# Performance work log

Hardware: AMD Instinct MI355X
Metric: run time of the kernel (lower is better)

The kernel has to match this reference:

```python
import jax, jax.numpy as jnp
import numpy as np

N, E, EDGES, G = 4096, 256, 131072, 64
H, DH = 4, 64  # MHA heads, head dim


def _ln(x, g, b, eps=1e-5):
    m = jnp.mean(x, -1, keepdims=True)
    v = jnp.var(x, -1, keepdims=True)
    return g * (x - m) * jax.lax.rsqrt(v + eps) + b


def setup_inputs() -> dict:
    key = jax.random.key(0)
    ks = jax.random.split(key, 40)
    i = iter(range(40))
    def rn(shape, s=1.0):
        return jax.random.normal(ks[next(i)], shape, jnp.float32) * s
    w = lambda shape: rn(shape, 0.02)
    inp = {
        "node_hidden": rn((N, E)),
        "edge_hidden": rn((EDGES, E)),
        "pos": rn((N, 3)),
        # GINEConv MLP: Lin(E,2E) -> LN -> ReLU -> Dropout -> Lin(2E,E)
        "gine_w1": w((E, 2 * E)), "gine_b1": jnp.zeros((2 * E,)),
        "gine_ln_g": jnp.ones((2 * E,)), "gine_ln_b": jnp.zeros((2 * E,)),
        "gine_w2": w((2 * E, E)), "gine_b2": jnp.zeros((E,)),
        "norm1_g": jnp.ones((E,)), "norm1_b": jnp.zeros((E,)),
        # DirectionalMessagePassing params
        "dir_w": w((3, E)), "dir_b": jnp.zeros((E,)),
        "msg_w": w((E, E)), "msg_b": jnp.zeros((E,)),
        # MultiheadAttention
        "wq": w((E, E)), "bq": jnp.zeros((E,)),
        "wk": w((E, E)), "bk": jnp.zeros((E,)),
        "wv": w((E, E)), "bv": jnp.zeros((E,)),
        "wo": w((E, E)), "bo": jnp.zeros((E,)),
        # gate
        "gate_w": w((2 * E, E)), "gate_b": jnp.zeros((E,)),
        "norm2_g": jnp.ones((E,)), "norm2_b": jnp.zeros((E,)),
        # GraphNorm affine
        "gn_g": jnp.ones((E,)), "gn_b": jnp.zeros((E,)),
        # int inputs
        "edge_index": jax.random.randint(ks[next(i)], (2, EDGES), 0, N, jnp.int64 if jax.config.jax_enable_x64 else jnp.int32),
        "node_id": jnp.sort(jax.random.randint(ks[next(i)], (N,), 0, G)),
        "edge_id": jax.random.randint(ks[next(i)], (EDGES,), 0, G),
    }
    return inp


def reference(node_hidden, edge_hidden, pos,
              gine_w1, gine_b1, gine_ln_g, gine_ln_b, gine_w2, gine_b2,
              norm1_g, norm1_b, dir_w, dir_b, msg_w, msg_b,
              wq, bq, wk, bk, wv, bv, wo, bo,
              gate_w, gate_b, norm2_g, norm2_b, gn_g, gn_b,
              edge_index, node_id, edge_id):
    src, dst = edge_index[0], edge_index[1]
    identity = node_hidden

    # --- GINEConv: out = MLP(x + sum_j relu(x_j + e_ij)), eps=0 ---
    msg = jax.nn.relu(node_hidden[src] + edge_hidden)           # [EDGES, E]
    agg = jax.ops.segment_sum(msg, dst, num_segments=N)         # [N, E]
    h = node_hidden + agg
    h = jax.nn.relu(_ln(h @ gine_w1 + gine_b1, gine_ln_g, gine_ln_b))
    gnn_out = _ln(h @ gine_w2 + gine_b2, norm1_g, norm1_b)      # norm1

    # --- DirectionalMessagePassing over unit edge directions ---
    vec = pos[dst] - pos[src]                                   # [EDGES, 3]
    vec = vec / (jnp.linalg.norm(vec, axis=-1, keepdims=True) + 1e-8)
    dfeat = vec @ dir_w + dir_b                                 # [EDGES, E]
    smsg = gnn_out[src] * dfeat
    sagg = jax.ops.segment_sum(smsg, dst, num_segments=N)
    spatial_out = sagg @ msg_w + msg_b                          # [N, E]

    # --- MHA: q = gnn_out, k = v = spatial_out (seq = nodes, batch=1) ---
    q = (gnn_out @ wq + bq).reshape(N, H, DH)
    k = (spatial_out @ wk + bk).reshape(N, H, DH)
    v = (spatial_out @ wv + bv).reshape(N, H, DH)
    scores = jnp.einsum("nhd,mhd->hnm", q, k) / np.sqrt(DH)
    attn = jax.nn.softmax(scores, axis=-1)
    fused = jnp.einsum("hnm,mhd->nhd", attn, v).reshape(N, E) @ wo + bo

    # --- gated residual blend + norm2 ---
    gate = jax.nn.sigmoid(jnp.concatenate([fused, identity], -1) @ gate_w + gate_b)
    out = gate * fused + (1.0 - gate) * identity
    out = _ln(out, norm2_g, norm2_b)

    # --- GraphNorm: per-graph mean/var over nodes (segment stats) ---
    counts = jax.ops.segment_sum(jnp.ones((N, 1), out.dtype), node_id, num_segments=G)
    mean = jax.ops.segment_sum(out, node_id, num_segments=G) / counts
    cen = out - mean[node_id]
    var = jax.ops.segment_sum(cen * cen, node_id, num_segments=G) / counts
    out = gn_g * cen * jax.lax.rsqrt(var[node_id] + 1e-5) + gn_b

    # last_act = True; dropout is eval-mode identity
    return jax.nn.relu(out)
```

## Files before the change

kernel.cpp:

```cpp
#include <hip/hip_runtime.h>
#include <hip/hip_bf16.h>

#define N_NODES 4096
#define E_DIM   256
#define N_EDGES 131072
#define N_GRAPHS 64
#define H_HEADS 4
#define DH      64
#define SPLIT   4

typedef unsigned short u16;
typedef __attribute__((ext_vector_type(8))) short bf16x8;
typedef __attribute__((ext_vector_type(4))) float f32x4;

__device__ __forceinline__ float u2f(u16 u) {
    union { unsigned int i; float f; } c; c.i = ((unsigned int)u) << 16; return c.f;
}
__device__ __forceinline__ u16 f2bu(float f) {
    __hip_bfloat16 h = __float2bfloat16(f);
    return *reinterpret_cast<u16*>(&h);
}
__device__ __forceinline__ float ldv(const void* p, size_t i, int f32) {
    return f32 ? ((const float*)p)[i] : u2f(((const u16*)p)[i]);
}
__device__ __forceinline__ float4 ldv4(const void* p, size_t i, int f32) {
    if (f32) return *(const float4*)((const float*)p + i);
    ushort4 u = *(const ushort4*)((const u16*)p + i);
    return make_float4(u2f(u.x), u2f(u.y), u2f(u.z), u2f(u.w));
}
__device__ __forceinline__ float4 ldb4(const u16* p, size_t i) {
    ushort4 u = *(const ushort4*)(p + i);
    return make_float4(u2f(u.x), u2f(u.y), u2f(u.z), u2f(u.w));
}
__device__ __forceinline__ int chk_f32(const void* ones_raw) { return ((const u16*)ones_raw)[0] == 0; }
__device__ __forceinline__ int chk_i64(const int* ei) {
    return (ei[1] == 0 && ei[3] == 0 && ei[5] == 0 && ei[7] == 0);
}
__device__ __forceinline__ int ldi(const int* p, int i, int i64) {
    return i64 ? p[2 * i] : p[i];
}

struct SmDesc { const void* src; float* dst; int n; };
struct SmTable { SmDesc d[18]; };
struct WtDesc { const void* src; u16* dst; int K; int N; int base; };
struct WtTable { WtDesc d[8]; };

__global__ __launch_bounds__(256) void k_prep(const void* __restrict__ x_r, float* __restrict__ xf,
                                              u16* __restrict__ xh, const void* __restrict__ pos_r,
                                              float4* __restrict__ pos4, SmTable st, WtTable wt,
                                              const void* __restrict__ msgw_r, u16* __restrict__ msgwb,
                                              const void* __restrict__ wo_r, u16* __restrict__ wob,
                                              const void* __restrict__ ones_raw) {
    __shared__ u16 tile[64][68];
    int b = blockIdx.x, t = threadIdx.x;
    int f32 = chk_f32(ones_raw);
    if (b < 4096) {
        int i = b * 256 + t;
        float v = ldv(x_r, i, f32);
        xf[i] = v; xh[i] = f2bu(v);
        return;
    }
    b -= 4096;
    if (b < 16) {
        int n = b * 256 + t;
        pos4[n] = make_float4(ldv(pos_r, n * 3 + 0, f32), ldv(pos_r, n * 3 + 1, f32),
                              ldv(pos_r, n * 3 + 2, f32), 0.f);
        return;
    }
    b -= 16;
    if (b < 18 * 48) {
        int ti = b / 48;
        int off = (b % 48) * 256 + t;
        SmDesc e = st.d[ti];
        if (off < e.n) e.dst[off] = ldv(e.src, off, f32);
        return;
    }
    b -= 18 * 48;
    if (b < 160) {
        int i = 0;
        while (i < 7 && b >= wt.d[i + 1].base) i++;
        WtDesc e = wt.d[i];
        int tl = b - e.base;
        int ntn = e.N >> 6;
        int kt = tl / ntn, nt = tl % ntn;
        int r = t >> 2, c0 = (t & 3) * 16;
#pragma unroll
        for (int j = 0; j < 16; j++)
            tile[r][c0 + j] = f2bu(ldv(e.src, (size_t)(kt * 64 + r) * e.N + nt * 64 + c0 + j, f32));
        __syncthreads();
#pragma unroll
        for (int j = 0; j < 16; j++)
            e.dst[(size_t)(nt * 64 + r) * e.K + kt * 64 + c0 + j] = tile[c0 + j][r];
        return;
    }
    b -= 160;
    if (b < 256) { int i = b * 256 + t; msgwb[i] = f2bu(ldv(msgw_r, i, f32)); return; }
    b -= 256;
    { int i = b * 256 + t; wob[i] = f2bu(ldv(wo_r, i, f32)); }
}

__global__ __launch_bounds__(256) void k_asm2(const u16* __restrict__ wot, const u16* __restrict__ foldT,
                                              const u16* __restrict__ gwt, u16* __restrict__ BT2) {
    int idx = blockIdx.x * 256 + threadIdx.x;
    int col = idx >> 9, k = idx & 511;
    u16 v;
    if (col < 256) v = (k < 256) ? wot[col * 256 + k] : (u16)0;
    else { int c = col - 256; v = (k < 256) ? foldT[c * 256 + k] : gwt[(size_t)c * 512 + k]; }
    BT2[idx] = v;
}

__global__ __launch_bounds__(256) void k_biases(const float* __restrict__ bqf, const float* __restrict__ bkf,
                                                const float* __restrict__ bvf, const float* __restrict__ msgbf,
                                                const u16* __restrict__ wkvt, const float* __restrict__ bof,
                                                const float* __restrict__ gbf, const u16* __restrict__ gwt,
                                                float* __restrict__ bqkv, float* __restrict__ bias2) {
    int b = blockIdx.x, t = threadIdx.x;
    if (b < 3) {
        int i = b * 256 + t;
        if (i < 256) { bqkv[i] = bqf[i]; return; }
        int c = i - 256;
        float s = (c < 256) ? bkf[c] : bvf[c - 256];
        const u16* row = wkvt + (size_t)c * 256;
        float acc = 0.f;
        for (int k = 0; k < 256; k++) acc = fmaf(msgbf[k], u2f(row[k]), acc);
        bqkv[256 + c] = s + acc;
    } else if (b == 3) {
        bias2[t] = bof[t];
    } else {
        float acc = gbf[t];
        const u16* row = gwt + (size_t)t * 512;
        for (int j = 0; j < 256; j++) acc = fmaf(bof[j], u2f(row[j]), acc);
        bias2[256 + t] = acc;
    }
}

__global__ __launch_bounds__(256) void k_mgemm(const void* __restrict__ A0, const void* __restrict__ A1,
                                               int as0, int as1, int abf0, int abf1,
                                               int K0, int Ktot, const u16* __restrict__ BT,
                                               const float* __restrict__ bias, void* __restrict__ C,
                                               int Nc, int outbf, int mode, u16* __restrict__ vt) {
    __shared__ u16 As[64 * 64];
    __shared__ u16 Bs[64 * 64];
    int t = threadIdx.x;
    int wv = t >> 6, l = t & 63, lg = l >> 4, lc = l & 15;
    int wm = wv >> 1, wn = wv & 1;
    int m0 = blockIdx.y * 64, n0 = blockIdx.x * 64;
    f32x4 acc[2][2] = {};
    int sr = t >> 2, sc = (t & 3) * 16;
    int sw = (sr & 7) << 3;

    for (int k0 = 0; k0 < Ktot; k0 += 64) {
        const void* Ab; int astr, kof, abf;
        if (mode == 1) { int pick = (n0 < K0); Ab = pick ? A0 : A1; astr = pick ? as0 : as1; abf = pick ? abf0 : abf1; kof = k0; }
        else if (k0 < K0) { Ab = A0; astr = as0; abf = abf0; kof = k0; }
        else { Ab = A1; astr = as1; abf = abf1; kof = k0 - K0; }
        if (abf) {
            const u16* Ap = (const u16*)Ab + (size_t)(m0 + sr) * astr + kof + sc;
            *(bf16x8*)&As[(sr * 64 + sc) ^ sw]     = *(const bf16x8*)Ap;
            *(bf16x8*)&As[(sr * 64 + sc + 8) ^ sw] = *(const bf16x8*)(Ap + 8);
        } else {
            const float* Ap = (const float*)Ab + (size_t)(m0 + sr) * astr + kof + sc;
#pragma unroll
            for (int j = 0; j < 2; j++) {
                float4 f0 = *(const float4*)(Ap + j * 8);
                float4 f1 = *(const float4*)(Ap + j * 8 + 4);
                bf16x8 bv;
                bv[0] = (short)f2bu(f0.x); bv[1] = (short)f2bu(f0.y);
                bv[2] = (short)f2bu(f0.z); bv[3] = (short)f2bu(f0.w);
                bv[4] = (short)f2bu(f1.x); bv[5] = (short)f2bu(f1.y);
                bv[6] = (short)f2bu(f1.z); bv[7] = (short)f2bu(f1.w);
                *(bf16x8*)&As[(sr * 64 + sc + j * 8) ^ sw] = bv;
            }
        }
        const u16* Bp = BT + (size_t)(n0 + sr) * Ktot + k0 + sc;
        *(bf16x8*)&Bs[(sr * 64 + sc) ^ sw]     = *(const bf16x8*)Bp;
        *(bf16x8*)&Bs[(sr * 64 + sc + 8) ^ sw] = *(const bf16x8*)(Bp + 8);
        __syncthreads();
#pragma unroll
        for (int ks = 0; ks < 2; ks++) {
            bf16x8 af[2], bfr[2];
#pragma unroll
            for (int mi = 0; mi < 2; mi++) {
                int row = wm * 32 + mi * 16 + lc;
                af[mi] = *(const bf16x8*)&As[(row * 64 + ks * 32 + lg * 8) ^ ((row & 7) << 3)];
            }
#pragma unroll
            for (int ni = 0; ni < 2; ni++) {
                int col = wn * 32 + ni * 16 + lc;
                bfr[ni] = *(const bf16x8*)&Bs[(col * 64 + ks * 32 + lg * 8) ^ ((col & 7) << 3)];
            }
#pragma unroll
            for (int mi = 0; mi < 2; mi++)
#pragma unroll
                for (int ni = 0; ni < 2; ni++)
                    acc[mi][ni] = __builtin_amdgcn_mfma_f32_16x16x32_bf16(af[mi], bfr[ni], acc[mi][ni], 0, 0, 0);
        }
        __syncthreads();
    }
#pragma unroll
    for (int mi = 0; mi < 2; mi++)
#pragma unroll
        for (int ni = 0; ni < 2; ni++) {
            int col = n0 + wn * 32 + ni * 16 + lc;
            float bb = bias ? bias[col] : 0.f;
#pragma unroll
            for (int r = 0; r < 4; r++) {
                int row = m0 + wm * 32 + mi * 16 + lg * 4 + r;
                float v = acc[mi][ni][r] + bb;
                u16 hb = f2bu(v);
                if (outbf) ((u16*)C)[(size_t)row * Nc + col] = hb;
                else       ((float*)C)[(size_t)row * Nc + col] = v;
                if (vt && col >= 512) vt[(size_t)(col - 512) * N_NODES + row] = hb;
            }
        }
}

__global__ __launch_bounds__(256) void k_attn(const u16* __restrict__ QKV, const u16* __restrict__ VT,
                                              u16* __restrict__ part) {
    __shared__ u16 K_lds[64 * 64];
    __shared__ u16 V_lds[64 * 64];
    __shared__ u16 P_lds[4][16 * 64];
    int t = threadIdx.x;
    int wv = t >> 6, l = t & 63;
    int lg = l >> 4, lc = l & 15;
    int h = blockIdx.y, c = blockIdx.z;
    int q0 = blockIdx.x * 64 + wv * 16;

    bf16x8 qf[2];
#pragma unroll
    for (int kk = 0; kk < 2; kk++)
        qf[kk] = *(const bf16x8*)&QKV[(size_t)(q0 + lc) * 768 + h * DH + kk * 32 + lg * 8];

    f32x4 oacc[4] = {};
    float mrow[4], lrow[4];
#pragma unroll
    for (int r = 0; r < 4; r++) { mrow[r] = -1e30f; lrow[r] = 0.f; }

    int lr = t >> 2, lc16 = (t & 3) * 16;

    for (int kv0 = c * (N_NODES / SPLIT); kv0 < (c + 1) * (N_NODES / SPLIT); kv0 += 64) {
        __syncthreads();
        {
            int base = lr * 64 + lc16;
            int sw = (lr & 7) << 3;
            const u16* kp = &QKV[(size_t)(kv0 + lr) * 768 + 256 + h * DH + lc16];
            *(bf16x8*)&K_lds[(base) ^ sw]     = *(const bf16x8*)kp;
            *(bf16x8*)&K_lds[(base + 8) ^ sw] = *(const bf16x8*)(kp + 8);
            const u16* vp = &VT[((size_t)h * DH + lr) * N_NODES + kv0 + lc16];
            *(bf16x8*)&V_lds[(base) ^ sw]     = *(const bf16x8*)vp;
            *(bf16x8*)&V_lds[(base + 8) ^ sw] = *(const bf16x8*)(vp + 8);
        }
        __syncthreads();

        f32x4 s[4];
#pragma unroll
        for (int n = 0; n < 4; n++) {
            f32x4 a = {};
#pragma unroll
            for (int kk = 0; kk < 2; kk++) {
                int row = n * 16 + lc;
                bf16x8 b = *(const bf16x8*)&K_lds[(row * 64 + kk * 32 + lg * 8) ^ ((row & 7) << 3)];
                a = __builtin_amdgcn_mfma_f32_16x16x32_bf16(qf[kk], b, a, 0, 0, 0);
            }
            s[n] = a;
        }
        float tm[4];
#pragma unroll
        for (int r = 0; r < 4; r++) {
#pragma unroll
            for (int n = 0; n < 4; n++) s[n][r] *= 0.125f;
            tm[r] = fmaxf(fmaxf(s[0][r], s[1][r]), fmaxf(s[2][r], s[3][r]));
        }
#pragma unroll
        for (int msk = 1; msk < 16; msk <<= 1)
#pragma unroll
            for (int r = 0; r < 4; r++) tm[r] = fmaxf(tm[r], __shfl_xor(tm[r], msk));

        float p[4][4], psum[4];
#pragma unroll
        for (int r = 0; r < 4; r++) {
            float nm = fmaxf(mrow[r], tm[r]);
            float alpha = __expf(mrow[r] - nm);
            lrow[r] *= alpha;
#pragma unroll
            for (int n = 0; n < 4; n++) oacc[n][r] *= alpha;
            float ps = 0.f;
#pragma unroll
            for (int n = 0; n < 4; n++) { p[n][r] = __expf(s[n][r] - nm); ps += p[n][r]; }
            psum[r] = ps;
            mrow[r] = nm;
        }
#pragma unroll
        for (int msk = 1; msk < 16; msk <<= 1)
#pragma unroll
            for (int r = 0; r < 4; r++) psum[r] += __shfl_xor(psum[r], msk);
#pragma unroll
        for (int r = 0; r < 4; r++) lrow[r] += psum[r];

#pragma unroll
        for (int r = 0; r < 4; r++) {
            int q = lg * 4 + r;
            int sw = (q & 7) << 3;
#pragma unroll
            for (int n = 0; n < 4; n++)
                P_lds[wv][(q * 64 + n * 16 + lc) ^ sw] = f2bu(p[n][r]);
        }
#pragma unroll
        for (int kc = 0; kc < 2; kc++) {
            bf16x8 a = *(const bf16x8*)&P_lds[wv][(lc * 64 + kc * 32 + lg * 8) ^ ((lc & 7) << 3)];
#pragma unroll
            for (int n = 0; n < 4; n++) {
                int row = n * 16 + lc;
                bf16x8 b = *(const bf16x8*)&V_lds[(row * 64 + kc * 32 + lg * 8) ^ ((row & 7) << 3)];
                oacc[n] = __builtin_amdgcn_mfma_f32_16x16x32_bf16(a, b, oacc[n], 0, 0, 0);
            }
        }
    }

#pragma unroll
    for (int r = 0; r < 4; r++) {
        u16* pp = part + ((size_t)(c * H_HEADS + h) * N_NODES + q0 + lg * 4 + r) * 72;
#pragma unroll
        for (int n = 0; n < 4; n++) pp[n * 16 + lc] = f2bu(oacc[n][r]);
        if (lc == 0) { *(float*)(pp + 64) = mrow[r]; *(float*)(pp + 66) = lrow[r]; }
    }
}

__global__ __launch_bounds__(256) void k_combine(const u16* __restrict__ part, u16* __restrict__ attnoh) {
    int n = blockIdx.x, t = threadIdx.x;
    int h = t >> 6, d = t & 63;
    float M = -1e30f;
#pragma unroll
    for (int c = 0; c < SPLIT; c++)
        M = fmaxf(M, *(const float*)(part + ((size_t)(c * H_HEADS + h) * N_NODES + n) * 72 + 64));
    float L = 0.f, o = 0.f;
#pragma unroll
    for (int c = 0; c < SPLIT; c++) {
        const u16* pp = part + ((size_t)(c * H_HEADS + h) * N_NODES + n) * 72;
        float w = __expf(*(const float*)(pp + 64) - M);
        L = fmaf(*(const float*)(pp + 66), w, L);
        o = fmaf(u2f(pp[d]), w, o);
    }
    attnoh[(size_t)n * E_DIM + h * DH + d] = f2bu(o / L);
}

__device__ __forceinline__ void block_red2(float& a, float& b, float* sbuf) {
#pragma unroll
    for (int o = 32; o > 0; o >>= 1) { a += __shfl_down(a, o); b += __shfl_down(b, o); }
    int w = threadIdx.x >> 6;
    if ((threadIdx.x & 63) == 0) { sbuf[w] = a; sbuf[4 + w] = b; }
    __syncthreads();
    a = sbuf[0] + sbuf[1] + sbuf[2] + sbuf[3];
    b = sbuf[4] + sbuf[5] + sbuf[6] + sbuf[7];
    __syncthreads();
}

__global__ void k_count(const int* __restrict__ ei, int* __restrict__ count) {
    int e = blockIdx.x * 256 + threadIdx.x;
    int i64 = chk_i64(ei);
    int d = i64 ? ei[2 * (N_EDGES + e)] : ei[N_EDGES + e];
    atomicAdd(&count[d], 1);
}

__global__ __launch_bounds__(1024) void k_scan(const int* __restrict__ count,
                                               int* __restrict__ offs, int* __restrict__ cursor) {
    __shared__ int wsum[16];
    int t = threadIdx.x, lane = t & 63, wid = t >> 6;
    int c0 = count[t * 4 + 0], c1 = count[t * 4 + 1], c2 = count[t * 4 + 2], c3 = count[t * 4 + 3];
    int tot = c0 + c1 + c2 + c3;
    int inc = tot;
#pragma unroll
    for (int o = 1; o < 64; o <<= 1) { int v = __shfl_up(inc, o); if (lane >= o) inc += v; }
    if (lane == 63) wsum[wid] = inc;
    __syncthreads();
    if (t < 16) {
        int v = wsum[t];
#pragma unroll
        for (int o = 1; o < 16; o <<= 1) { int u = __shfl_up(v, o); if (t >= o) v += u; }
        wsum[t] = v;
    }
    __syncthreads();
    int base = (wid ? wsum[wid - 1] : 0) + inc - tot;
    int o0 = base, o1 = base + c0, o2 = o1 + c1, o3 = o2 + c2;
    offs[t * 4 + 0] = o0; offs[t * 4 + 1] = o1; offs[t * 4 + 2] = o2; offs[t * 4 + 3] = o3;
    cursor[t * 4 + 0] = o0; cursor[t * 4 + 1] = o1; cursor[t * 4 + 2] = o2; cursor[t * 4 + 3] = o3;
    if (t == 1023) offs[4096] = wsum[15];
}

__global__ void k_scatter(const int* __restrict__ ei, int* __restrict__ cursor,
                          int2* __restrict__ elist2) {
    int e = blockIdx.x * 256 + threadIdx.x;
    int i64 = chk_i64(ei);
    int s = i64 ? ei[2 * e] : ei[e];
    int d = i64 ? ei[2 * (N_EDGES + e)] : ei[N_EDGES + e];
    int p = atomicAdd(&cursor[d], 1);
    elist2[p] = make_int2(e, s);
}

__global__ __launch_bounds__(256) void k_gine_agg(const float* __restrict__ xf, const u16* __restrict__ xh,
                                                  const void* __restrict__ eh, const void* __restrict__ ones_raw,
                                                  const int* __restrict__ offs, const int2* __restrict__ elist2,
                                                  u16* __restrict__ houth) {
    int wv = threadIdx.x >> 6, ld = threadIdx.x & 63;
    int n = blockIdx.x * 4 + wv;
    int f32 = chk_f32(ones_raw);
    int cc = ld * 4;
    float4 acc = *(const float4*)&xf[(size_t)n * E_DIM + cc];
    int i0 = offs[n], i1 = offs[n + 1];
    int i = i0;
    for (; i + 4 <= i1; i += 4) {
        int2 es[4];
#pragma unroll
        for (int j = 0; j < 4; j++) es[j] = elist2[i + j];
        float4 a[4], x[4];
#pragma unroll
        for (int j = 0; j < 4; j++) a[j] = ldv4(eh, (size_t)es[j].x * E_DIM + cc, f32);
#pragma unroll
        for (int j = 0; j < 4; j++) x[j] = ldb4(xh, (size_t)es[j].y * E_DIM + cc);
#pragma unroll
        for (int j = 0; j < 4; j++) {
            acc.x += fmaxf(x[j].x + a[j].x, 0.f);
            acc.y += fmaxf(x[j].y + a[j].y, 0.f);
            acc.z += fmaxf(x[j].z + a[j].z, 0.f);
            acc.w += fmaxf(x[j].w + a[j].w, 0.f);
        }
    }
    for (; i < i1; i++) {
        int2 es = elist2[i];
        float4 a0 = ldv4(eh, (size_t)es.x * E_DIM + cc, f32);
        float4 x0 = ldb4(xh, (size_t)es.y * E_DIM + cc);
        acc.x += fmaxf(x0.x + a0.x, 0.f);
        acc.y += fmaxf(x0.y + a0.y, 0.f);
        acc.z += fmaxf(x0.z + a0.z, 0.f);
        acc.w += fmaxf(x0.w + a0.w, 0.f);
    }
    ushort4 o;
    o.x = f2bu(acc.x); o.y = f2bu(acc.y); o.z = f2bu(acc.z); o.w = f2bu(acc.w);
    *(ushort4*)&houth[(size_t)n * E_DIM + cc] = o;
}

template <int W, int OUTBF>
__global__ __launch_bounds__(256) void k_ln(const float* __restrict__ in, void* __restrict__ out,
                                            const float* __restrict__ g, const float* __restrict__ b,
                                            int relu) {
    __shared__ float sbuf[8];
    constexpr int PE = W / 256;
    int n = blockIdx.x, t = threadIdx.x;
    const float* row = in + (size_t)n * W;
    float x[PE];
    float s = 0.f, s2 = 0.f;
#pragma unroll
    for (int i = 0; i < PE; i++) { x[i] = row[t + i * 256]; s += x[i]; s2 += x[i] * x[i]; }
    block_red2(s, s2, sbuf);
    float mean = s / W;
    float var = fmaxf(s2 / W - mean * mean, 0.f);
    float rstd = rsqrtf(var + 1e-5f);
#pragma unroll
    for (int i = 0; i < PE; i++) {
        int c = t + i * 256;
        float y = g[c] * (x[i] - mean) * rstd + b[c];
        if (relu) y = fmaxf(y, 0.f);
        if (OUTBF) ((u16*)out)[(size_t)n * W + c] = f2bu(y);
        else       ((float*)out)[(size_t)n * W + c] = y;
    }
}

__global__ __launch_bounds__(256) void k_dir(const float4* __restrict__ pos4, const int* __restrict__ offs,
                                             const int2* __restrict__ elist2, const u16* __restrict__ gnnh,
                                             const float* __restrict__ dw, const float* __restrict__ db,
                                             u16* __restrict__ saggh) {
    int wv = threadIdx.x >> 6, ld = threadIdx.x & 63;
    int n = blockIdx.x * 4 + wv;
    int cc = ld * 4;
    float4 w0 = *(const float4*)&dw[cc];
    float4 w1 = *(const float4*)&dw[256 + cc];
    float4 w2 = *(const float4*)&dw[512 + cc];
    float4 bb = *(const float4*)&db[cc];
    float4 pn = pos4[n];
    float4 acc = {0.f, 0.f, 0.f, 0.f};
    int i0 = offs[n], i1 = offs[n + 1];
    int i = i0;
    for (; i + 2 <= i1; i += 2) {
        int2 es0 = elist2[i], es1 = elist2[i + 1];
        float4 p0 = pos4[es0.y], p1 = pos4[es1.y];
        float4 g0 = ldb4(gnnh, (size_t)es0.y * E_DIM + cc);
        float4 g1 = ldb4(gnnh, (size_t)es1.y * E_DIM + cc);
        float vx0 = pn.x - p0.x, vy0 = pn.y - p0.y, vz0 = pn.z - p0.z;
        float vx1 = pn.x - p1.x, vy1 = pn.y - p1.y, vz1 = pn.z - p1.z;
        float rn0 = 1.f / (sqrtf(vx0 * vx0 + vy0 * vy0 + vz0 * vz0) + 1e-8f);
        float rn1 = 1.f / (sqrtf(vx1 * vx1 + vy1 * vy1 + vz1 * vz1) + 1e-8f);
        acc.x = fmaf(g0.x, bb.x + (vx0 * w0.x + vy0 * w1.x + vz0 * w2.x) * rn0, acc.x);
        acc.y = fmaf(g0.y, bb.y + (vx0 * w0.y + vy0 * w1.y + vz0 * w2.y) * rn0, acc.y);
        acc.z = fmaf(g0.z, bb.z + (vx0 * w0.z + vy0 * w1.z + vz0 * w2.z) * rn0, acc.z);
        acc.w = fmaf(g0.w, bb.w + (vx0 * w0.w + vy0 * w1.w + vz0 * w2.w) * rn0, acc.w);
        acc.x = fmaf(g1.x, bb.x + (vx1 * w0.x + vy1 * w1.x + vz1 * w2.x) * rn1, acc.x);
        acc.y = fmaf(g1.y, bb.y + (vx1 * w0.y + vy1 * w1.y + vz1 * w2.y) * rn1, acc.y);
        acc.z = fmaf(g1.z, bb.z + (vx1 * w0.z + vy1 * w1.z + vz1 * w2.z) * rn1, acc.z);
        acc.w = fmaf(g1.w, bb.w + (vx1 * w0.w + vy1 * w1.w + vz1 * w2.w) * rn1, acc.w);
    }
    if (i < i1) {
        int2 es0 = elist2[i];
        float4 p0 = pos4[es0.y];
        float4 g0 = ldb4(gnnh, (size_t)es0.y * E_DIM + cc);
        float vx0 = pn.x - p0.x, vy0 = pn.y - p0.y, vz0 = pn.z - p0.z;
        float rn0 = 1.f / (sqrtf(vx0 * vx0 + vy0 * vy0 + vz0 * vz0) + 1e-8f);
        acc.x = fmaf(g0.x, bb.x + (vx0 * w0.x + vy0 * w1.x + vz0 * w2.x) * rn0, acc.x);
        acc.y = fmaf(g0.y, bb.y + (vx0 * w0.y + vy0 * w1.y + vz0 * w2.y) * rn0, acc.y);
        acc.z = fmaf(g0.z, bb.z + (vx0 * w0.z + vy0 * w1.z + vz0 * w2.z) * rn0, acc.z);
        acc.w = fmaf(g0.w, bb.w + (vx0 * w0.w + vy0 * w1.w + vz0 * w2.w) * rn0, acc.w);
    }
    ushort4 o;
    o.x = f2bu(acc.x); o.y = f2bu(acc.y); o.z = f2bu(acc.z); o.w = f2bu(acc.w);
    *(ushort4*)&saggh[(size_t)n * E_DIM + cc] = o;
}

__global__ __launch_bounds__(256) void k_gate_ln(const float* __restrict__ fg, const float* __restrict__ xf,
                                                 const float* __restrict__ g2, const float* __restrict__ b2,
                                                 float* __restrict__ out2) {
    __shared__ float sbuf[8];
    int n = blockIdx.x, t = threadIdx.x;
    float fu = fg[(size_t)n * 512 + t];
    float z  = fg[(size_t)n * 512 + 256 + t];
    float gate = 1.f / (1.f + __expf(-z));
    float o = gate * fu + (1.f - gate) * xf[(size_t)n * E_DIM + t];
    float s = o, s2 = o * o;
    block_red2(s, s2, sbuf);
    float mean = s / E_DIM;
    float var = fmaxf(s2 / E_DIM - mean * mean, 0.f);
    float y = g2[t] * (o - mean) * rsqrtf(var + 1e-5f) + b2[t];
    out2[(size_t)n * E_DIM + t] = y;
}

__device__ __forceinline__ int lbound(const int* __restrict__ nid, int v, int i64) {
    int lo = 0, hi = N_NODES;
    while (lo < hi) { int mid = (lo + hi) >> 1; if (ldi(nid, mid, i64) < v) lo = mid + 1; else hi = mid; }
    return lo;
}

__global__ __launch_bounds__(256) void k_gnstats(const int* __restrict__ nid, const int* __restrict__ ei,
                                                 const float* __restrict__ out2,
                                                 float* __restrict__ gnm, float* __restrict__ gnr) {
    int g = blockIdx.x, t = threadIdx.x;
    int i64 = chk_i64(ei);
    int a = lbound(nid, g, i64), bnd = lbound(nid, g + 1, i64);
    int cnt = bnd - a;
    float s = 0.f, s2 = 0.f;
    for (int n = a; n < bnd; n++) {
        float x = out2[(size_t)n * E_DIM + t];
        s += x; s2 = fmaf(x, x, s2);
    }
    float inv = cnt ? 1.f / (float)cnt : 0.f;
    float mean = s * inv;
    float var = fmaxf(s2 * inv - mean * mean, 0.f);
    gnm[g * E_DIM + t] = mean;
    gnr[g * E_DIM + t] = rsqrtf(var + 1e-5f);
}

__global__ __launch_bounds__(256) void k_gnapply(const float* __restrict__ out2, const int* __restrict__ nid,
                                                 const int* __restrict__ ei, const void* __restrict__ ones_raw,
                                                 const float* __restrict__ gnm, const float* __restrict__ gnr,
                                                 const float* __restrict__ gg, const float* __restrict__ gb,
                                                 void* __restrict__ out) {
    int n = blockIdx.x, t = threadIdx.x;
    int g = ldi(nid, n, chk_i64(ei));
    float y = gg[t] * (out2[(size_t)n * E_DIM + t] - gnm[g * E_DIM + t]) * gnr[g * E_DIM + t] + gb[t];
    y = fmaxf(y, 0.f);
    size_t idx = (size_t)n * E_DIM + t;
    if (chk_f32(ones_raw)) ((float*)out)[idx] = y;
    else ((__hip_bfloat16*)out)[idx] = __float2bfloat16(y);
}

extern "C" void kernel_launch(void* const* d_in, const int* in_sizes, int n_in,
                              void* d_out, int out_size, void* d_ws, size_t ws_size,
                              hipStream_t stream) {
    const void* x_r    = d_in[0];
    const void* eh_r   = d_in[1];
    const void* pos_r  = d_in[2];
    const void* w1_r   = d_in[3];
    const void* b1_r   = d_in[4];
    const void* glng_r = d_in[5];
    const void* glnb_r = d_in[6];
    const void* w2_r   = d_in[7];
    const void* b2_r   = d_in[8];
    const void* n1g_r  = d_in[9];
    const void* n1b_r  = d_in[10];
    const void* dirw_r = d_in[11];
    const void* dirb_r = d_in[12];
    const void* msgw_r = d_in[13];
    const void* msgb_r = d_in[14];
    const void* wq_r   = d_in[15];
    const void* bq_r   = d_in[16];
    const void* wk_r   = d_in[17];
    const void* bk_r   = d_in[18];
    const void* wv_r   = d_in[19];
    const void* bv_r   = d_in[20];
    const void* wo_r   = d_in[21];
    const void* bo_r   = d_in[22];
    const void* gw_r   = d_in[23];
    const void* gb_r   = d_in[24];
    const void* n2g_r  = d_in[25];
    const void* n2b_r  = d_in[26];
    const void* gng_r  = d_in[27];
    const void* gnb_r  = d_in[28];
    const int* ei      = (const int*)d_in[29];
    const int* nid     = (const int*)d_in[30];

    char* ws = (char*)d_ws;
    const size_t KB = 1 << 10, MB = 1 << 20;
    int*   count  = (int*)(ws + 0);
    int*   offs   = (int*)(ws + 32 * KB);
    int*   cursor = (int*)(ws + 64 * KB);
    int2*  elist2 = (int2*)(ws + 128 * KB);

    float* prm    = (float*)(ws + 1 * MB + 192 * KB);
    float* b1f   = prm + 0;
    float* glngf = prm + 512,  *glnbf = prm + 1024;
    float* b2f   = prm + 1536;
    float* n1gf  = prm + 1792, *n1bf  = prm + 2048;
    float* dirwf = prm + 2304;
    float* dirbf = prm + 3072, *msgbf = prm + 3328;
    float* bqf   = prm + 3584, *bkf   = prm + 3840, *bvf = prm + 4096, *bof = prm + 4352;
    float* gbf   = prm + 4608;
    float* n2gf  = prm + 4864, *n2bf  = prm + 5120;
    float* gngf  = prm + 5376, *gnbf  = prm + 5632;
    float4* pos4 = (float4*)(ws + 1 * MB + 256 * KB);

    u16* w1t    = (u16*)(ws + 2 * MB);
    u16* w2t    = (u16*)(ws + 2 * MB + 256 * KB);
    u16* wot    = (u16*)(ws + 2 * MB + 512 * KB);
    u16* gwt    = (u16*)(ws + 2 * MB + 640 * KB);
    u16* wqkvt  = (u16*)(ws + 3 * MB);
    u16* wkvt   = (u16*)(ws + 3 * MB + 384 * KB);
    u16* msgwb  = (u16*)(ws + 3 * MB + 640 * KB);
    u16* wob    = (u16*)(ws + 3 * MB + 768 * KB);
    u16* foldT  = (u16*)(ws + 3 * MB + 896 * KB);
    u16* BT2    = (u16*)(ws + 4 * MB);
    float* bias2f = (float*)(ws + 4 * MB + 512 * KB);
    float* bqkvf  = (float*)(ws + 4 * MB + 516 * KB);

    float* xf     = (float*)(ws + 5 * MB);
    u16*   xh     = (u16*)(ws + 9 * MB);
    u16*   hbufh  = (u16*)(ws + 11 * MB);
    float* T1     = (float*)(ws + 13 * MB);
    float* gnnf   = (float*)(ws + 21 * MB);
    u16*   gnnh   = (u16*)(ws + 25 * MB);
    u16*   saggh  = (u16*)(ws + 27 * MB);
    u16*   QKVh   = (u16*)(ws + 29 * MB);
    u16*   VT     = (u16*)(ws + 35 * MB);
    u16*   part   = (u16*)(ws + 37 * MB);
    u16*   attnoh = (u16*)(ws + 11 * MB);
    float* fg     = (float*)(ws + 13 * MB);
    float* out2   = (float*)(ws + 21 * MB);
    float* gnm    = (float*)(ws + 25 * MB);
    float* gnr    = (float*)(ws + 25 * MB + 64 * KB);

    SmTable st;
    {
        int i = 0;
        auto add = [&](const void* s, float* d, int n) { st.d[i].src = s; st.d[i].dst = d; st.d[i].n = n; i++; };
        add(b1_r, b1f, 512); add(glng_r, glngf, 512); add(glnb_r, glnbf, 512);
        add(b2_r, b2f, 256); add(n1g_r, n1gf, 256); add(n1b_r, n1bf, 256);
        add(dirw_r, dirwf, 768); add(dirb_r, dirbf, 256); add(msgb_r, msgbf, 256);
        add(bq_r, bqf, 256); add(bk_r, bkf, 256); add(bv_r, bvf, 256); add(bo_r, bof, 256);
        add(gb_r, gbf, 256); add(n2g_r, n2gf, 256); add(n2b_r, n2bf, 256);
        add(gng_r, gngf, 256); add(gnb_r, gnbf, 256);
    }
    WtTable wt;
    {
        int i = 0, base = 0;
        auto add = [&](const void* s, u16* d, int K, int N) {
            wt.d[i].src = s; wt.d[i].dst = d; wt.d[i].K = K; wt.d[i].N = N; wt.d[i].base = base;
            base += (K / 64) * (N / 64); i++;
        };
        add(w1_r, w1t, 256, 512);
        add(w2_r, w2t, 512, 256);
        add(wq_r, wqkvt, 256, 256);
        add(wk_r, wkvt, 256, 256);
        add(wv_r, wkvt + 256 * 256, 256, 256);
        add(wo_r, wot, 256, 256);
        add(gw_r, gwt, 512, 256);
        wt.d[7].base = 0x7fffffff;
    }
    k_prep<<<4096 + 16 + 18 * 48 + 160 + 256 + 256, 256, 0, stream>>>(
        x_r, xf, xh, pos_r, pos4, st, wt, msgw_r, msgwb, wo_r, wob, glng_r);

    hipMemsetAsync(count, 0, N_NODES * sizeof(int), stream);
    k_count<<<N_EDGES / 256, 256, 0, stream>>>(ei, count);
    k_scan<<<1, 1024, 0, stream>>>(count, offs, cursor);
    k_scatter<<<N_EDGES / 256, 256, 0, stream>>>(ei, cursor, elist2);

    k_mgemm<<<dim3(4, 8), 256, 0, stream>>>(wkvt, nullptr, 256, 0, 1, 0, 256, 256, msgwb,
                                            nullptr, wqkvt + 256 * 256, 256, 1, 0, nullptr);
    k_mgemm<<<dim3(4, 4), 256, 0, stream>>>(gwt, nullptr, 512, 0, 1, 0, 256, 256, wob,
                                            nullptr, foldT, 256, 1, 0, nullptr);
    k_asm2<<<1024, 256, 0, stream>>>(wot, foldT, gwt, BT2);
    k_biases<<<5, 256, 0, stream>>>(bqf, bkf, bvf, msgbf, wkvt, bof, gbf, gwt, bqkvf, bias2f);

    k_gine_agg<<<N_NODES / 4, 256, 0, stream>>>(xf, xh, eh_r, glng_r, offs, elist2, hbufh);
    k_mgemm<<<dim3(8, 64), 256, 0, stream>>>(hbufh, nullptr, 256, 0, 1, 0, 256, 256, w1t,
                                             b1f, T1, 512, 0, 0, nullptr);
    k_ln<512, 0><<<N_NODES, 256, 0, stream>>>(T1, T1, glngf, glnbf, 1);
    k_mgemm<<<dim3(4, 64), 256, 0, stream>>>(T1, nullptr, 512, 0, 0, 0, 512, 512, w2t,
                                             b2f, gnnf, 256, 0, 0, nullptr);
    k_ln<256, 1><<<N_NODES, 256, 0, stream>>>(gnnf, gnnh, n1gf, n1bf, 0);

    k_dir<<<N_NODES / 4, 256, 0, stream>>>(pos4, offs, elist2, gnnh, dirwf, dirbf, saggh);

    k_mgemm<<<dim3(12, 64), 256, 0, stream>>>(gnnh, saggh, 256, 256, 1, 1, 256, 256, wqkvt,
                                              bqkvf, QKVh, 768, 1, 1, VT);

    k_attn<<<dim3(N_NODES / 64, H_HEADS, SPLIT), 256, 0, stream>>>(QKVh, VT, part);
    k_combine<<<N_NODES, 256, 0, stream>>>(part, attnoh);

    k_mgemm<<<dim3(8, 64), 256, 0, stream>>>(attnoh, xf, 256, 256, 1, 0, 256, 512, BT2,
                                             bias2f, fg, 512, 0, 0, nullptr);
    k_gate_ln<<<N_NODES, 256, 0, stream>>>(fg, xf, n2gf, n2bf, out2);

    k_gnstats<<<N_GRAPHS, 256, 0, stream>>>(nid, ei, out2, gnm, gnr);
    k_gnapply<<<N_NODES, 256, 0, stream>>>(out2, nid, ei, glng_r, gnm, gnr, gngf, gnbf, d_out);
}
```

Baseline: 269.4 us.

## Restructure attention softmax, split GraphNorm stats, and merge small setup launches

The attention kernel swaps the MFMA operand order so each lane holds a full query column. Row max and sum then reduce with two shuffles instead of four, and the softmax uses exp2 with log2e folded into the scale. GraphNorm statistics are split into 8 chunks per graph, giving 512 blocks in place of 64, and the apply kernel sums the partials itself. The count memset is folded into the prep kernel, and the asm2 and biases kernels are merged into one launch, which cuts launch overhead at the cost of extra per-node partial reads.

Result: faster. 262.7 us (-2.5%).

```diff
diff --git a/kernel.cpp b/kernel.cpp
--- a/kernel.cpp
+++ b/kernel.cpp
@@ -50,7 +50,7 @@
                                               float4* __restrict__ pos4, SmTable st, WtTable wt,
                                               const void* __restrict__ msgw_r, u16* __restrict__ msgwb,
                                               const void* __restrict__ wo_r, u16* __restrict__ wob,
-                                              const void* __restrict__ ones_raw) {
+                                              int* __restrict__ count, const void* __restrict__ ones_raw) {
     __shared__ u16 tile[64][68];
     int b = blockIdx.x, t = threadIdx.x;
     int f32 = chk_f32(ones_raw);
@@ -96,25 +96,29 @@
     b -= 160;
     if (b < 256) { int i = b * 256 + t; msgwb[i] = f2bu(ldv(msgw_r, i, f32)); return; }
     b -= 256;
-    { int i = b * 256 + t; wob[i] = f2bu(ldv(wo_r, i, f32)); }
-}
-
-__global__ __launch_bounds__(256) void k_asm2(const u16* __restrict__ wot, const u16* __restrict__ foldT,
-                                              const u16* __restrict__ gwt, u16* __restrict__ BT2) {
-    int idx = blockIdx.x * 256 + threadIdx.x;
-    int col = idx >> 9, k = idx & 511;
-    u16 v;
-    if (col < 256) v = (k < 256) ? wot[col * 256 + k] : (u16)0;
-    else { int c = col - 256; v = (k < 256) ? foldT[c * 256 + k] : gwt[(size_t)c * 512 + k]; }
-    BT2[idx] = v;
-}
-
-__global__ __launch_bounds__(256) void k_biases(const float* __restrict__ bqf, const float* __restrict__ bkf,
-                                                const float* __restrict__ bvf, const float* __restrict__ msgbf,
-                                                const u16* __restrict__ wkvt, const float* __restrict__ bof,
-                                                const float* __restrict__ gbf, const u16* __restrict__ gwt,
-                                                float* __restrict__ bqkv, float* __restrict__ bias2) {
+    if (b < 256) { int i = b * 256 + t; wob[i] = f2bu(ldv(wo_r, i, f32)); return; }
+    b -= 256;
+    count[b * 256 + t] = 0;
+}
+
+__global__ __launch_bounds__(256) void k_post(const u16* __restrict__ wot, const u16* __restrict__ foldT,
+                                              const u16* __restrict__ gwt, u16* __restrict__ BT2,
+                                              const float* __restrict__ bqf, const float* __restrict__ bkf,
+                                              const float* __restrict__ bvf, const float* __restrict__ msgbf,
+                                              const u16* __restrict__ wkvt, const float* __restrict__ bof,
+                                              const float* __restrict__ gbf,
+                                              float* __restrict__ bqkv, float* __restrict__ bias2) {
     int b = blockIdx.x, t = threadIdx.x;
+    if (b < 1024) {
+        int idx = b * 256 + t;
+        int col = idx >> 9, k = idx & 511;
+        u16 v;
+        if (col < 256) v = (k < 256) ? wot[col * 256 + k] : (u16)0;
+        else { int c = col - 256; v = (k < 256) ? foldT[c * 256 + k] : gwt[(size_t)c * 512 + k]; }
+        BT2[idx] = v;
+        return;
+    }
+    b -= 1024;
     if (b < 3) {
         int i = b * 256 + t;
         if (i < 256) { bqkv[i] = bqf[i]; return; }
@@ -225,6 +229,7 @@
     int lg = l >> 4, lc = l & 15;
     int h = blockIdx.y, c = blockIdx.z;
     int q0 = blockIdx.x * 64 + wv * 16;
+    const float SC = 0.18033688f;
 
     bf16x8 qf[2];
 #pragma unroll
@@ -232,11 +237,10 @@
         qf[kk] = *(const bf16x8*)&QKV[(size_t)(q0 + lc) * 768 + h * DH + kk * 32 + lg * 8];
 
     f32x4 oacc[4] = {};
-    float mrow[4], lrow[4];
-#pragma unroll
-    for (int r = 0; r < 4; r++) { mrow[r] = -1e30f; lrow[r] = 0.f; }
+    float mx = -1e30f, lsum = 0.f;
 
     int lr = t >> 2, lc16 = (t & 3) * 16;
+    int swp = (lc & 7) << 3;
 
     for (int kv0 = c * (N_NODES / SPLIT); kv0 < (c + 1) * (N_NODES / SPLIT); kv0 += 64) {
         __syncthreads();
@@ -259,55 +263,46 @@
 #pragma unroll
             for (int kk = 0; kk < 2; kk++) {
                 int row = n * 16 + lc;
-                bf16x8 b = *(const bf16x8*)&K_lds[(row * 64 + kk * 32 + lg * 8) ^ ((row & 7) << 3)];
-                a = __builtin_amdgcn_mfma_f32_16x16x32_bf16(qf[kk], b, a, 0, 0, 0);
+                bf16x8 kf = *(const bf16x8*)&K_lds[(row * 64 + kk * 32 + lg * 8) ^ ((row & 7) << 3)];
+                a = __builtin_amdgcn_mfma_f32_16x16x32_bf16(kf, qf[kk], a, 0, 0, 0);
             }
             s[n] = a;
         }
-        float tm[4];
-#pragma unroll
-        for (int r = 0; r < 4; r++) {
-#pragma unroll
-            for (int n = 0; n < 4; n++) s[n][r] *= 0.125f;
-            tm[r] = fmaxf(fmaxf(s[0][r], s[1][r]), fmaxf(s[2][r], s[3][r]));
-        }
-#pragma unroll
-        for (int msk = 1; msk < 16; msk <<= 1)
-#pragma unroll
-            for (int r = 0; r < 4; r++) tm[r] = fmaxf(tm[r], __shfl_xor(tm[r], msk));
-
-        float p[4][4], psum[4];
-#pragma unroll
-        for (int r = 0; r < 4; r++) {
-            float nm = fmaxf(mrow[r], tm[r]);
-            float alpha = __expf(mrow[r] - nm);
-            lrow[r] *= alpha;
-#pragma unroll
-            for (int n = 0; n < 4; n++) oacc[n][r] *= alpha;
-            float ps = 0.f;
-#pragma unroll
-            for (int n = 0; n < 4; n++) { p[n][r] = __expf(s[n][r] - nm); ps += p[n][r]; }
-            psum[r] = ps;
-            mrow[r] = nm;
-        }
-#pragma unroll
-        for (int msk = 1; msk < 16; msk <<= 1)
-#pragma unroll
-            for (int r = 0; r < 4; r++) psum[r] += __shfl_xor(psum[r], msk);
-#pragma unroll
-        for (int r = 0; r < 4; r++) lrow[r] += psum[r];
-
-#pragma unroll
-        for (int r = 0; r < 4; r++) {
-            int q = lg * 4 + r;
-            int sw = (q & 7) << 3;
-#pragma unroll
-            for (int n = 0; n < 4; n++)
-                P_lds[wv][(q * 64 + n * 16 + lc) ^ sw] = f2bu(p[n][r]);
-        }
+        float tm = -1e30f;
+#pragma unroll
+        for (int n = 0; n < 4; n++)
+#pragma unroll
+            for (int r = 0; r < 4; r++) { s[n][r] *= SC; tm = fmaxf(tm, s[n][r]); }
+        tm = fmaxf(tm, __shfl_xor(tm, 16));
+        tm = fmaxf(tm, __shfl_xor(tm, 32));
+        float nm = fmaxf(mx, tm);
+        float alpha = exp2f(mx - nm);
+        mx = nm;
+        float p[4][4], ps = 0.f;
+#pragma unroll
+        for (int n = 0; n < 4; n++)
+#pragma unroll
+            for (int r = 0; r < 4; r++) { p[n][r] = exp2f(s[n][r] - nm); ps += p[n][r]; }
+        ps += __shfl_xor(ps, 16);
+        ps += __shfl_xor(ps, 32);
+        lsum = lsum * alpha + ps;
+
+        float af[4];
+#pragma unroll
+        for (int r = 0; r < 4; r++) af[r] = __shfl(alpha, lg * 4 + r);
+#pragma unroll
+        for (int n = 0; n < 4; n++)
+#pragma unroll
+            for (int r = 0; r < 4; r++) oacc[n][r] *= af[r];
+
+#pragma unroll
+        for (int n = 0; n < 4; n++)
+#pragma unroll
+            for (int r = 0; r < 4; r++)
+                P_lds[wv][(lc * 64 + n * 16 + lg * 4 + r) ^ swp] = f2bu(p[n][r]);
 #pragma unroll
         for (int kc = 0; kc < 2; kc++) {
-            bf16x8 a = *(const bf16x8*)&P_lds[wv][(lc * 64 + kc * 32 + lg * 8) ^ ((lc & 7) << 3)];
+            bf16x8 a = *(const bf16x8*)&P_lds[wv][(lc * 64 + kc * 32 + lg * 8) ^ swp];
 #pragma unroll
             for (int n = 0; n < 4; n++) {
                 int row = n * 16 + lc;
@@ -317,12 +312,18 @@
         }
     }
 
+    float lf[4], mf[4];
+#pragma unroll
+    for (int r = 0; r < 4; r++) {
+        lf[r] = __shfl(lsum, lg * 4 + r);
+        mf[r] = __shfl(mx, lg * 4 + r);
+    }
 #pragma unroll
     for (int r = 0; r < 4; r++) {
         u16* pp = part + ((size_t)(c * H_HEADS + h) * N_NODES + q0 + lg * 4 + r) * 72;
 #pragma unroll
         for (int n = 0; n < 4; n++) pp[n * 16 + lc] = f2bu(oacc[n][r]);
-        if (lc == 0) { *(float*)(pp + 64) = mrow[r]; *(float*)(pp + 66) = lrow[r]; }
+        if (lc == 0) { *(float*)(pp + 64) = mf[r]; *(float*)(pp + 66) = lf[r]; }
     }
 }
 
@@ -337,7 +338,7 @@
 #pragma unroll
     for (int c = 0; c < SPLIT; c++) {
         const u16* pp = part + ((size_t)(c * H_HEADS + h) * N_NODES + n) * 72;
-        float w = __expf(*(const float*)(pp + 64) - M);
+        float w = exp2f(*(const float*)(pp + 64) - M);
         L = fmaf(*(const float*)(pp + 66), w, L);
         o = fmaf(u2f(pp[d]), w, o);
     }
@@ -538,32 +539,40 @@
 }
 
 __global__ __launch_bounds__(256) void k_gnstats(const int* __restrict__ nid, const int* __restrict__ ei,
-                                                 const float* __restrict__ out2,
-                                                 float* __restrict__ gnm, float* __restrict__ gnr) {
-    int g = blockIdx.x, t = threadIdx.x;
+                                                 const float* __restrict__ out2, float* __restrict__ gnp) {
+    int g = blockIdx.x >> 3, ch = blockIdx.x & 7, t = threadIdx.x;
     int i64 = chk_i64(ei);
-    int a = lbound(nid, g, i64), bnd = lbound(nid, g + 1, i64);
-    int cnt = bnd - a;
+    int a = lbound(nid, g, i64), b = lbound(nid, g + 1, i64);
+    int len = b - a;
+    int s0 = a + (len * ch) / 8, s1 = a + (len * (ch + 1)) / 8;
     float s = 0.f, s2 = 0.f;
-    for (int n = a; n < bnd; n++) {
+    for (int n = s0; n < s1; n++) {
         float x = out2[(size_t)n * E_DIM + t];
         s += x; s2 = fmaf(x, x, s2);
     }
-    float inv = cnt ? 1.f / (float)cnt : 0.f;
-    float mean = s * inv;
-    float var = fmaxf(s2 * inv - mean * mean, 0.f);
-    gnm[g * E_DIM + t] = mean;
-    gnr[g * E_DIM + t] = rsqrtf(var + 1e-5f);
+    gnp[((size_t)(g * 8 + ch) * 2 + 0) * 256 + t] = s;
+    gnp[((size_t)(g * 8 + ch) * 2 + 1) * 256 + t] = s2;
 }
 
 __global__ __launch_bounds__(256) void k_gnapply(const float* __restrict__ out2, const int* __restrict__ nid,
                                                  const int* __restrict__ ei, const void* __restrict__ ones_raw,
-                                                 const float* __restrict__ gnm, const float* __restrict__ gnr,
+                                                 const float* __restrict__ gnp,
                                                  const float* __restrict__ gg, const float* __restrict__ gb,
                                                  void* __restrict__ out) {
     int n = blockIdx.x, t = threadIdx.x;
-    int g = ldi(nid, n, chk_i64(ei));
-    float y = gg[t] * (out2[(size_t)n * E_DIM + t] - gnm[g * E_DIM + t]) * gnr[g * E_DIM + t] + gb[t];
+    int i64 = chk_i64(ei);
+    int g = ldi(nid, n, i64);
+    int a = lbound(nid, g, i64), b = lbound(nid, g + 1, i64);
+    float inv = 1.f / (float)(b - a);
+    float s = 0.f, s2 = 0.f;
+#pragma unroll
+    for (int ch = 0; ch < 8; ch++) {
+        s  += gnp[((size_t)(g * 8 + ch) * 2 + 0) * 256 + t];
+        s2 += gnp[((size_t)(g * 8 + ch) * 2 + 1) * 256 + t];
+    }
+    float mean = s * inv;
+    float var = fmaxf(s2 * inv - mean * mean, 0.f);
+    float y = gg[t] * (out2[(size_t)n * E_DIM + t] - mean) * rsqrtf(var + 1e-5f) + gb[t];
     y = fmaxf(y, 0.f);
     size_t idx = (size_t)n * E_DIM + t;
     if (chk_f32(ones_raw)) ((float*)out)[idx] = y;
@@ -651,8 +660,7 @@
     u16*   attnoh = (u16*)(ws + 11 * MB);
     float* fg     = (float*)(ws + 13 * MB);
     float* out2   = (float*)(ws + 21 * MB);
-    float* gnm    = (float*)(ws + 25 * MB);
-    float* gnr    = (float*)(ws + 25 * MB + 64 * KB);
+    float* gnp    = (float*)(ws + 25 * MB);
 
     SmTable st;
     {
@@ -681,10 +689,9 @@
         add(gw_r, gwt, 512, 256);
         wt.d[7].base = 0x7fffffff;
     }
-    k_prep<<<4096 + 16 + 18 * 48 + 160 + 256 + 256, 256, 0, stream>>>(
-        x_r, xf, xh, pos_r, pos4, st, wt, msgw_r, msgwb, wo_r, wob, glng_r);
-
-    hipMemsetAsync(count, 0, N_NODES * sizeof(int), stream);
+    k_prep<<<4096 + 16 + 18 * 48 + 160 + 256 + 256 + 16, 256, 0, stream>>>(
+        x_r, xf, xh, pos_r, pos4, st, wt, msgw_r, msgwb, wo_r, wob, count, glng_r);
+
     k_count<<<N_EDGES / 256, 256, 0, stream>>>(ei, count);
     k_scan<<<1, 1024, 0, stream>>>(count, offs, cursor);
     k_scatter<<<N_EDGES / 256, 256, 0, stream>>>(ei, cursor, elist2);
@@ -693,8 +700,8 @@
                                             nullptr, wqkvt + 256 * 256, 256, 1, 0, nullptr);
     k_mgemm<<<dim3(4, 4), 256, 0, stream>>>(gwt, nullptr, 512, 0, 1, 0, 256, 256, wob,
                                             nullptr, foldT, 256, 1, 0, nullptr);
-    k_asm2<<<1024, 256, 0, stream>>>(wot, foldT, gwt, BT2);
-    k_biases<<<5, 256, 0, stream>>>(bqf, bkf, bvf, msgbf, wkvt, bof, gbf, gwt, bqkvf, bias2f);
+    k_post<<<1029, 256, 0, stream>>>(wot, foldT, gwt, BT2, bqf, bkf, bvf, msgbf, wkvt,
+                                     bof, gbf, bqkvf, bias2f);
 
     k_gine_agg<<<N_NODES / 4, 256, 0, stream>>>(xf, xh, eh_r, glng_r, offs, elist2, hbufh);
     k_mgemm<<<dim3(8, 64), 256, 0, stream>>>(hbufh, nullptr, 256, 0, 1, 0, 256, 256, w1t,
@@ -716,6 +723,6 @@
                                              bias2f, fg, 512, 0, 0, nullptr);
     k_gate_ln<<<N_NODES, 256, 0, stream>>>(fg, xf, n2gf, n2bf, out2);
 
-    k_gnstats<<<N_GRAPHS, 256, 0, stream>>>(nid, ei, out2, gnm, gnr);
-    k_gnapply<<<N_NODES, 256, 0, stream>>>(out2, nid, ei, glng_r, gnm, gnr, gngf, gnbf, d_out);
-}
+    k_gnstats<<<N_GRAPHS * 8, 256, 0, stream>>>(nid, ei, out2, gnp);
+    k_gnapply<<<N_NODES, 256, 0, stream>>>(out2, nid, ei, glng_r, gnp, gngf, gnbf, d_out);
+}
```
